# Performance work log

Measured on AMD Instinct MI355X. Metric: run time of the kernel, lower is better.

Reference implementation:

```python
import jax, jax.numpy as jnp
import numpy as np

N_NODES = 100000
N_EDGES = 1600000
IN_DIM = 128
HID = 64
NEG_SLOPE = 0.01  # F.leaky_relu default


def setup_inputs() -> dict:
    key = jax.random.key(0)
    ks = jax.random.split(key, 8)
    h = jax.random.normal(ks[0], (N_NODES, IN_DIM), dtype=jnp.float32)
    edge_index = jax.random.randint(ks[1], (2, N_EDGES), 0, N_NODES, dtype=jnp.int32)
    s1 = 1.0 / np.sqrt(IN_DIM)
    s2 = 1.0 / np.sqrt(HID)
    W1a = jax.random.normal(ks[2], (IN_DIM, HID), dtype=jnp.float32) * s1
    b1a = jnp.zeros((HID,), dtype=jnp.float32)
    W1b = jax.random.normal(ks[3], (HID, HID), dtype=jnp.float32) * s2
    b1b = jnp.zeros((HID,), dtype=jnp.float32)
    W2a = jax.random.normal(ks[4], (HID, HID), dtype=jnp.float32) * s2
    b2a = jnp.zeros((HID,), dtype=jnp.float32)
    W2b = jax.random.normal(ks[5], (HID, HID), dtype=jnp.float32) * s2
    b2b = jnp.zeros((HID,), dtype=jnp.float32)
    return dict(h=h, edge_index=edge_index, W1a=W1a, b1a=b1a, W1b=W1b, b1b=b1b,
                W2a=W2a, b2a=b2a, W2b=W2b, b2b=b2b)


def _gin_layer(h, src, dst, Wa, ba, Wb, bb):
    # sum aggregation over incoming edges: agg[v] = sum_{(u->v)} h[u]
    agg = jax.ops.segment_sum(h[src], dst, num_segments=N_NODES)
    z = h + agg  # (1 + eps) * h + agg, eps = 0 (learn_eps=False)
    z = jax.nn.relu(z @ Wa + ba) @ Wb + bb  # 2-layer MLP
    return jax.nn.leaky_relu(z, NEG_SLOPE)


def reference(h, edge_index, W1a, b1a, W1b, b1b, W2a, b2a, W2b, b2b):
    src, dst = edge_index[0], edge_index[1]
    h = _gin_layer(h, src, dst, W1a, b1a, W1b, b1b)
    h = _gin_layer(h, src, dst, W2a, b2a, W2b, b2b)
    return h
```

## Files before the change

### kernel.cpp

```cpp
#include <hip/hip_runtime.h>

#define IN_DIM 128
#define HID 64
#define NEG 0.01f
#define NBUCK 512
#define EPT 16

typedef unsigned int uint;
typedef unsigned short u16;
typedef __attribute__((ext_vector_type(8))) short s8v;
typedef __attribute__((ext_vector_type(4))) float f4v;

__device__ __forceinline__ float blo(uint u) { return __uint_as_float(u << 16); }
__device__ __forceinline__ float bhi(uint u) { return __uint_as_float(u & 0xffff0000u); }
__device__ __forceinline__ u16 bf16r(float x) {
    uint u = __float_as_uint(x);
    u = (u + 0x7fffu + ((u >> 16) & 1u)) >> 16;
    return (u16)u;
}
__device__ __forceinline__ uint bfpair(float a, float b) {
    uint ua = __float_as_uint(a), ub = __float_as_uint(b);
    ua = (ua + 0x7fffu + ((ua >> 16) & 1u)) >> 16;
    ub = (ub + 0x7fffu + ((ub >> 16) & 1u)) & 0xffff0000u;
    return ua | ub;
}
__device__ __forceinline__ s8v pack8(float4 x, float4 y) {
    uint4 qq = make_uint4(bfpair(x.x, x.y), bfpair(x.z, x.w),
                          bfpair(y.x, y.y), bfpair(y.z, y.w));
    return *reinterpret_cast<s8v*>(&qq);
}

__global__ __launch_bounds__(256) void prep_frags(const float* __restrict__ W1a,
                                                  const float* __restrict__ W1b,
                                                  const float* __restrict__ W2a,
                                                  const float* __restrict__ W2b,
                                                  u16* __restrict__ wf,
                                                  int* __restrict__ gcnt) {
    int t = threadIdx.x;
    for (int i = t; i < NBUCK; i += 256) gcnt[i] = 0;
    for (int task = t; task < 40 * 64; task += 256) {
        int f = task >> 6, l = task & 63;
        const float* W;
        int kt, nt;
        if (f < 16)      { W = W1a; kt = f & 3;        nt = f >> 2; }
        else if (f < 24) { W = W1b; kt = (f - 16) & 1; nt = (f - 16) >> 1; }
        else if (f < 32) { W = W2a; kt = (f - 24) & 1; nt = (f - 24) >> 1; }
        else             { W = W2b; kt = (f - 32) & 1; nt = (f - 32) >> 1; }
        int col = nt * 16 + (l & 15);
        int k0  = kt * 32 + (l >> 4) * 8;
        for (int j = 0; j < 8; ++j)
            wf[f * 512 + l * 8 + j] = bf16r(W[(k0 + j) * HID + col]);
    }
}

__global__ __launch_bounds__(256) void proj_hist(const float* __restrict__ h,
                                                 const u16* __restrict__ wf,
                                                 u16* __restrict__ pout, int M,
                                                 const int* __restrict__ dst,
                                                 int* __restrict__ gcnt,
                                                 int nE, int B, int histB) {
    if ((int)blockIdx.x < histB) {
        __shared__ int lc[NBUCK];
        for (int i = threadIdx.x; i < NBUCK; i += 256) lc[i] = 0;
        __syncthreads();
        int idx = blockIdx.x * 256 + threadIdx.x;
        int stride = histB * 256;
        for (int e = idx; e < nE; e += stride) atomicAdd(&lc[dst[e] >> 8], 1);
        __syncthreads();
        for (int i = threadIdx.x; i < B; i += 256) {
            int c = lc[i];
            if (c) atomicAdd(&gcnt[i], c);
        }
    } else {
        int wid = threadIdx.x >> 6, lane = threadIdx.x & 63;
        int lr = lane & 15, kg = lane >> 4;
        int node0 = ((int)blockIdx.x - histB) * 64 + wid * 16;
        s8v bfr[16];
#pragma unroll
        for (int f = 0; f < 16; ++f)
            bfr[f] = *reinterpret_cast<const s8v*>(wf + f * 512 + lane * 8);
        f4v zero = {0.f, 0.f, 0.f, 0.f};
        f4v acc[4] = {zero, zero, zero, zero};
        int nodeA = min(node0 + lr, M - 1);
        const float* hp = h + (size_t)nodeA * IN_DIM + kg * 8;
#pragma unroll
        for (int kt = 0; kt < 4; ++kt) {
            float4 x = *reinterpret_cast<const float4*>(hp + kt * 32);
            float4 y = *reinterpret_cast<const float4*>(hp + kt * 32 + 4);
            s8v afr = pack8(x, y);
#pragma unroll
            for (int nt = 0; nt < 4; ++nt)
                acc[nt] = __builtin_amdgcn_mfma_f32_16x16x32_bf16(afr, bfr[nt * 4 + kt], acc[nt], 0, 0, 0);
        }
#pragma unroll
        for (int jj = 0; jj < 4; ++jj) {
            int node = node0 + kg * 4 + jj;
            if (node < M) {
#pragma unroll
                for (int nt = 0; nt < 4; ++nt)
                    pout[(size_t)node * HID + nt * 16 + lr] = bf16r(acc[nt][jj]);
            }
        }
    }
}

__global__ __launch_bounds__(256) void coarse_scan(const int* __restrict__ gcnt,
                                                   int* __restrict__ bbase,
                                                   int* __restrict__ bcur) {
    __shared__ int sc[NBUCK];
    int t = threadIdx.x;
    sc[t] = gcnt[t];
    sc[t + 256] = gcnt[t + 256];
    __syncthreads();
    for (int off = 1; off < NBUCK; off <<= 1) {
        int x0 = sc[t], x1 = sc[t + 256];
        int y0 = (t >= off) ? sc[t - off] : 0;
        int y1 = (t + 256 >= off) ? sc[t + 256 - off] : 0;
        __syncthreads();
        sc[t] = x0 + y0;
        sc[t + 256] = x1 + y1;
        __syncthreads();
    }
    int e0 = (t == 0) ? 0 : sc[t - 1];
    int e1 = sc[t + 255];
    bbase[t] = e0;        bcur[t] = e0;
    bbase[t + 256] = e1;  bcur[t + 256] = e1;
}

__global__ __launch_bounds__(256) void partition(const int* __restrict__ src,
                                                 const int* __restrict__ dst,
                                                 int* __restrict__ bcur,
                                                 uint* __restrict__ ebuf,
                                                 int nE, int nRounds) {
    __shared__ int rcnt[NBUCK];
    __shared__ int chunk[NBUCK];
    int t = threadIdx.x;
    for (int r = blockIdx.x; r < nRounds; r += gridDim.x) {
        int base = r * (EPT * 256);
        for (int i = t; i < NBUCK; i += 256) rcnt[i] = 0;
        __syncthreads();
        uint pk[EPT];
        int rb[EPT];
#pragma unroll
        for (int j = 0; j < EPT; ++j) {
            int e = base + j * 256 + t;
            rb[j] = -1;
            if (e < nE) {
                int d = dst[e];
                int b = d >> 8;
                pk[j] = (uint)src[e] | ((uint)(d & 255) << 24);
                int rk = atomicAdd(&rcnt[b], 1);
                rb[j] = (rk << 9) | b;
            }
        }
        __syncthreads();
        for (int i = t; i < NBUCK; i += 256) {
            int c = rcnt[i];
            if (c) chunk[i] = atomicAdd(&bcur[i], c);
        }
        __syncthreads();
#pragma unroll
        for (int j = 0; j < EPT; ++j) {
            if (rb[j] >= 0) {
                int b = rb[j] & 511, rk = rb[j] >> 9;
                ebuf[chunk[b] + rk] = pk[j];
            }
        }
        __syncthreads();
    }
}

__global__ __launch_bounds__(256) void bucket_csr(const uint* __restrict__ ebuf,
                                                  const int* __restrict__ bbase,
                                                  const int* __restrict__ bcur,
                                                  int* __restrict__ rp,
                                                  int* __restrict__ ssrc,
                                                  int M, int nE) {
    __shared__ int cnt[256], sc[256], cur[256];
    int b = blockIdx.x, t = threadIdx.x;
    int ebeg = bbase[b], eend = bcur[b];
    cnt[t] = 0;
    __syncthreads();
    for (int e = ebeg + t; e < eend; e += 256) atomicAdd(&cnt[ebuf[e] >> 24], 1);
    __syncthreads();
    sc[t] = cnt[t];
    __syncthreads();
    for (int off = 1; off < 256; off <<= 1) {
        int x = sc[t];
        int y = (t >= off) ? sc[t - off] : 0;
        __syncthreads();
        sc[t] = x + y;
        __syncthreads();
    }
    int excl = (t == 0) ? 0 : sc[t - 1];
    int node = (b << 8) + t;
    if (node < M) rp[node] = ebeg + excl;
    if (b == 0 && t == 0) rp[M] = nE;
    cur[t] = excl;
    __syncthreads();
    for (int e = ebeg + t; e < eend; e += 256) {
        uint u = ebuf[e];
        int r = atomicAdd(&cur[u >> 24], 1);
        ssrc[ebeg + r] = (int)(u & 0x00ffffffu);
    }
}

__global__ __launch_bounds__(256, 8) void gather_z(const uint* __restrict__ pin,
                                                   const int* __restrict__ rp,
                                                   const int* __restrict__ ssrc,
                                                   const float* __restrict__ ba,
                                                   uint* __restrict__ zout, int M) {
    int lane = threadIdx.x & 63;
    int half = lane >> 5, col = lane & 31;
    int wave = (blockIdx.x * 256 + threadIdx.x) >> 6;
    int nW = gridDim.x * 4;
    for (int v = wave; v < M; v += nW) {
        int beg = rp[v], end = rp[v + 1];
        float f0 = 0.f, f1 = 0.f;
        for (int cb = beg; cb < end; cb += 64) {
            int n = min(64, end - cb);
            int eid = (lane < n) ? ssrc[cb + lane] : 0;
            int j = 0;
            for (; j + 16 <= n; j += 16) {
                int s0 = __shfl(eid, j + 0 + half);
                int s1 = __shfl(eid, j + 2 + half);
                int s2 = __shfl(eid, j + 4 + half);
                int s3 = __shfl(eid, j + 6 + half);
                int s4 = __shfl(eid, j + 8 + half);
                int s5 = __shfl(eid, j + 10 + half);
                int s6 = __shfl(eid, j + 12 + half);
                int s7 = __shfl(eid, j + 14 + half);
                uint u0 = pin[(size_t)s0 * 32 + col];
                uint u1 = pin[(size_t)s1 * 32 + col];
                uint u2 = pin[(size_t)s2 * 32 + col];
                uint u3 = pin[(size_t)s3 * 32 + col];
                uint u4 = pin[(size_t)s4 * 32 + col];
                uint u5 = pin[(size_t)s5 * 32 + col];
                uint u6 = pin[(size_t)s6 * 32 + col];
                uint u7 = pin[(size_t)s7 * 32 + col];
                f0 += (blo(u0) + blo(u1)) + (blo(u2) + blo(u3))
                    + (blo(u4) + blo(u5)) + (blo(u6) + blo(u7));
                f1 += (bhi(u0) + bhi(u1)) + (bhi(u2) + bhi(u3))
                    + (bhi(u4) + bhi(u5)) + (bhi(u6) + bhi(u7));
            }
            for (; j + 8 <= n; j += 8) {
                int s0 = __shfl(eid, j + 0 + half);
                int s1 = __shfl(eid, j + 2 + half);
                int s2 = __shfl(eid, j + 4 + half);
                int s3 = __shfl(eid, j + 6 + half);
                uint u0 = pin[(size_t)s0 * 32 + col];
                uint u1 = pin[(size_t)s1 * 32 + col];
                uint u2 = pin[(size_t)s2 * 32 + col];
                uint u3 = pin[(size_t)s3 * 32 + col];
                f0 += (blo(u0) + blo(u1)) + (blo(u2) + blo(u3));
                f1 += (bhi(u0) + bhi(u1)) + (bhi(u2) + bhi(u3));
            }
            for (; j < n; j += 2) {
                int idx = j + half;
                int s = __shfl(eid, idx);
                uint u = 0;
                if (idx < n) u = pin[(size_t)s * 32 + col];
                f0 += blo(u);
                f1 += bhi(u);
            }
        }
        f0 += __shfl_xor(f0, 32);
        f1 += __shfl_xor(f1, 32);
        uint us = pin[(size_t)v * 32 + col];
        f0 += blo(us);
        f1 += bhi(us);
        float2 vb = ((const float2*)ba)[col];
        f0 = fmaxf(f0 + vb.x, 0.f);
        f1 = fmaxf(f1 + vb.y, 0.f);
        if (lane < 32) zout[(size_t)v * 32 + col] = bfpair(f0, f1);
    }
}

template<bool HAS_NEXT>
__global__ __launch_bounds__(256) void mlp_mfma(const u16* __restrict__ zin,
                                                const u16* __restrict__ wfb,
                                                const float* __restrict__ bb,
                                                const u16* __restrict__ wfn,
                                                u16* __restrict__ pout,
                                                float* __restrict__ fout, int M) {
    int wid = threadIdx.x >> 6, lane = threadIdx.x & 63;
    int lr = lane & 15, kg = lane >> 4;
    int node0 = blockIdx.x * 64 + wid * 16;
    s8v bfr[8];
#pragma unroll
    for (int f = 0; f < 8; ++f)
        bfr[f] = *reinterpret_cast<const s8v*>(wfb + f * 512 + lane * 8);
    f4v zero = {0.f, 0.f, 0.f, 0.f};
    f4v acc[4] = {zero, zero, zero, zero};
    int nodeA = min(node0 + lr, M - 1);
    const u16* zp = zin + (size_t)nodeA * HID + kg * 8;
#pragma unroll
    for (int kt = 0; kt < 2; ++kt) {
        s8v afr = *reinterpret_cast<const s8v*>(zp + kt * 32);
#pragma unroll
        for (int nt = 0; nt < 4; ++nt)
            acc[nt] = __builtin_amdgcn_mfma_f32_16x16x32_bf16(afr, bfr[nt * 2 + kt], acc[nt], 0, 0, 0);
    }
    float h1[4][4];
#pragma unroll
    for (int nt = 0; nt < 4; ++nt) {
        float b = bb[nt * 16 + lr];
#pragma unroll
        for (int jj = 0; jj < 4; ++jj) {
            float v = acc[nt][jj] + b;
            h1[nt][jj] = (v > 0.f) ? v : v * NEG;
        }
    }
    if constexpr (!HAS_NEXT) {
#pragma unroll
        for (int jj = 0; jj < 4; ++jj) {
            int node = node0 + kg * 4 + jj;
            if (node < M) {
#pragma unroll
                for (int nt = 0; nt < 4; ++nt)
                    fout[(size_t)node * HID + nt * 16 + lr] = h1[nt][jj];
            }
        }
    } else {
        __shared__ float tls[4][16][68];
#pragma unroll
        for (int nt = 0; nt < 4; ++nt)
#pragma unroll
            for (int jj = 0; jj < 4; ++jj)
                tls[wid][kg * 4 + jj][nt * 16 + lr] = h1[nt][jj];
        s8v wfr[8];
#pragma unroll
        for (int f = 0; f < 8; ++f)
            wfr[f] = *reinterpret_cast<const s8v*>(wfn + f * 512 + lane * 8);
        f4v acc2[4] = {zero, zero, zero, zero};
#pragma unroll
        for (int kt = 0; kt < 2; ++kt) {
            float4 x = *reinterpret_cast<const float4*>(&tls[wid][lr][kt * 32 + kg * 8]);
            float4 y = *reinterpret_cast<const float4*>(&tls[wid][lr][kt * 32 + kg * 8 + 4]);
            s8v afr = pack8(x, y);
#pragma unroll
            for (int nt = 0; nt < 4; ++nt)
                acc2[nt] = __builtin_amdgcn_mfma_f32_16x16x32_bf16(afr, wfr[nt * 2 + kt], acc2[nt], 0, 0, 0);
        }
#pragma unroll
        for (int jj = 0; jj < 4; ++jj) {
            int node = node0 + kg * 4 + jj;
            if (node < M) {
#pragma unroll
                for (int nt = 0; nt < 4; ++nt)
                    pout[(size_t)node * HID + nt * 16 + lr] = bf16r(acc2[nt][jj]);
            }
        }
    }
}

extern "C" void kernel_launch(void* const* d_in, const int* in_sizes, int n_in,
                              void* d_out, int out_size, void* d_ws, size_t ws_size,
                              hipStream_t stream) {
    const float* h   = (const float*)d_in[0];
    const int*   ei  = (const int*)d_in[1];
    const float* W1a = (const float*)d_in[2];
    const float* b1a = (const float*)d_in[3];
    const float* W1b = (const float*)d_in[4];
    const float* b1b = (const float*)d_in[5];
    const float* W2a = (const float*)d_in[6];
    const float* b2a = (const float*)d_in[7];
    const float* W2b = (const float*)d_in[8];
    const float* b2b = (const float*)d_in[9];

    int M  = in_sizes[0] / IN_DIM;
    int nE = in_sizes[1] / 2;
    const int* src = ei;
    const int* dst = ei + nE;

    int B = (M + 255) >> 8;

    uint*  p1    = (uint*)d_ws;
    uint*  p2    = p1 + (size_t)M * 32;
    uint*  z     = p2 + (size_t)M * 32;
    int*   gcnt  = (int*)(z + (size_t)M * 32);
    int*   bbase = gcnt + NBUCK;
    int*   bcur  = bbase + NBUCK;
    int*   rp    = bcur + NBUCK;
    int*   ssrc  = rp + (M + 1);
    uint*  ebuf  = (uint*)(ssrc + nE);
    u16*   wf    = (u16*)(ebuf + nE);

    int gB = 2048;
    int mB = (M + 63) / 64;
    int histB = 160;
    int nRounds = (nE + EPT * 256 - 1) / (EPT * 256);

    prep_frags<<<1, 256, 0, stream>>>(W1a, W1b, W2a, W2b, wf, gcnt);

    proj_hist<<<histB + mB, 256, 0, stream>>>(h, wf, (u16*)p1, M, dst, gcnt, nE, B, histB);

    coarse_scan<<<1, 256, 0, stream>>>(gcnt, bbase, bcur);
    partition<<<nRounds, 256, 0, stream>>>(src, dst, bcur, ebuf, nE, nRounds);
    bucket_csr<<<B, 256, 0, stream>>>(ebuf, bbase, bcur, rp, ssrc, M, nE);

    gather_z<<<gB, 256, 0, stream>>>(p1, rp, ssrc, b1a, z, M);
    mlp_mfma<true><<<mB, 256, 0, stream>>>((const u16*)z, wf + 16 * 512, b1b, wf + 24 * 512,
                                           (u16*)p2, nullptr, M);
    gather_z<<<gB, 256, 0, stream>>>(p2, rp, ssrc, b2a, z, M);
    mlp_mfma<false><<<mB, 256, 0, stream>>>((const u16*)z, wf + 32 * 512, b2b, nullptr,
                                            nullptr, (float*)d_out, M);
}
```

Measured before the change: 163.6 us.

## Gather with 8 lanes per node using 16-byte loads instead of one wave per node

Restructures the CSR gather so each wave handles 8 nodes, with 8 lanes per node each loading a uint4 (8 bf16 features) per neighbor. Indices are read directly per lane instead of being staged and broadcast with shuffles. The grid grows to one thread per 8 features of every node rather than a grid-stride loop. This cuts shuffle overhead and per-wave serialization over low-degree nodes and issues wider loads, at the cost of divergence between nodes of different degree within a wave.

```diff
diff --git a/kernel.cpp b/kernel.cpp
--- a/kernel.cpp
+++ b/kernel.cpp
@@ -211,69 +211,56 @@
                                                    const float* __restrict__ ba,
                                                    uint* __restrict__ zout, int M) {
     int lane = threadIdx.x & 63;
-    int half = lane >> 5, col = lane & 31;
-    int wave = (blockIdx.x * 256 + threadIdx.x) >> 6;
-    int nW = gridDim.x * 4;
-    for (int v = wave; v < M; v += nW) {
-        int beg = rp[v], end = rp[v + 1];
-        float f0 = 0.f, f1 = 0.f;
-        for (int cb = beg; cb < end; cb += 64) {
-            int n = min(64, end - cb);
-            int eid = (lane < n) ? ssrc[cb + lane] : 0;
-            int j = 0;
-            for (; j + 16 <= n; j += 16) {
-                int s0 = __shfl(eid, j + 0 + half);
-                int s1 = __shfl(eid, j + 2 + half);
-                int s2 = __shfl(eid, j + 4 + half);
-                int s3 = __shfl(eid, j + 6 + half);
-                int s4 = __shfl(eid, j + 8 + half);
-                int s5 = __shfl(eid, j + 10 + half);
-                int s6 = __shfl(eid, j + 12 + half);
-                int s7 = __shfl(eid, j + 14 + half);
-                uint u0 = pin[(size_t)s0 * 32 + col];
-                uint u1 = pin[(size_t)s1 * 32 + col];
-                uint u2 = pin[(size_t)s2 * 32 + col];
-                uint u3 = pin[(size_t)s3 * 32 + col];
-                uint u4 = pin[(size_t)s4 * 32 + col];
-                uint u5 = pin[(size_t)s5 * 32 + col];
-                uint u6 = pin[(size_t)s6 * 32 + col];
-                uint u7 = pin[(size_t)s7 * 32 + col];
-                f0 += (blo(u0) + blo(u1)) + (blo(u2) + blo(u3))
-                    + (blo(u4) + blo(u5)) + (blo(u6) + blo(u7));
-                f1 += (bhi(u0) + bhi(u1)) + (bhi(u2) + bhi(u3))
-                    + (bhi(u4) + bhi(u5)) + (bhi(u6) + bhi(u7));
-            }
-            for (; j + 8 <= n; j += 8) {
-                int s0 = __shfl(eid, j + 0 + half);
-                int s1 = __shfl(eid, j + 2 + half);
-                int s2 = __shfl(eid, j + 4 + half);
-                int s3 = __shfl(eid, j + 6 + half);
-                uint u0 = pin[(size_t)s0 * 32 + col];
-                uint u1 = pin[(size_t)s1 * 32 + col];
-                uint u2 = pin[(size_t)s2 * 32 + col];
-                uint u3 = pin[(size_t)s3 * 32 + col];
-                f0 += (blo(u0) + blo(u1)) + (blo(u2) + blo(u3));
-                f1 += (bhi(u0) + bhi(u1)) + (bhi(u2) + bhi(u3));
-            }
-            for (; j < n; j += 2) {
-                int idx = j + half;
-                int s = __shfl(eid, idx);
-                uint u = 0;
-                if (idx < n) u = pin[(size_t)s * 32 + col];
-                f0 += blo(u);
-                f1 += bhi(u);
-            }
-        }
-        f0 += __shfl_xor(f0, 32);
-        f1 += __shfl_xor(f1, 32);
-        uint us = pin[(size_t)v * 32 + col];
-        f0 += blo(us);
-        f1 += bhi(us);
-        float2 vb = ((const float2*)ba)[col];
-        f0 = fmaxf(f0 + vb.x, 0.f);
-        f1 = fmaxf(f1 + vb.y, 0.f);
-        if (lane < 32) zout[(size_t)v * 32 + col] = bfpair(f0, f1);
-    }
+    int g = lane >> 3, q = lane & 7;
+    int w = (blockIdx.x * 256 + threadIdx.x) >> 6;
+    int v = w * 8 + g;
+    if (v >= M) return;
+    const uint4* pin4 = (const uint4*)pin;
+    int beg = rp[v], end = rp[v + 1];
+    uint4 u = pin4[(size_t)v * 8 + q];
+    float f0 = blo(u.x), f1 = bhi(u.x), f2 = blo(u.y), f3 = bhi(u.y);
+    float f4 = blo(u.z), f5 = bhi(u.z), f6 = blo(u.w), f7 = bhi(u.w);
+    int e = beg;
+    for (; e + 4 <= end; e += 4) {
+        int s0 = ssrc[e], s1 = ssrc[e + 1], s2 = ssrc[e + 2], s3 = ssrc[e + 3];
+        uint4 a = pin4[(size_t)s0 * 8 + q];
+        uint4 b = pin4[(size_t)s1 * 8 + q];
+        uint4 c = pin4[(size_t)s2 * 8 + q];
+        uint4 d = pin4[(size_t)s3 * 8 + q];
+        f0 += (blo(a.x) + blo(b.x)) + (blo(c.x) + blo(d.x));
+        f1 += (bhi(a.x) + bhi(b.x)) + (bhi(c.x) + bhi(d.x));
+        f2 += (blo(a.y) + blo(b.y)) + (blo(c.y) + blo(d.y));
+        f3 += (bhi(a.y) + bhi(b.y)) + (bhi(c.y) + bhi(d.y));
+        f4 += (blo(a.z) + blo(b.z)) + (blo(c.z) + blo(d.z));
+        f5 += (bhi(a.z) + bhi(b.z)) + (bhi(c.z) + bhi(d.z));
+        f6 += (blo(a.w) + blo(b.w)) + (blo(c.w) + blo(d.w));
+        f7 += (bhi(a.w) + bhi(b.w)) + (bhi(c.w) + bhi(d.w));
+    }
+    for (; e + 2 <= end; e += 2) {
+        int s0 = ssrc[e], s1 = ssrc[e + 1];
+        uint4 a = pin4[(size_t)s0 * 8 + q];
+        uint4 b = pin4[(size_t)s1 * 8 + q];
+        f0 += blo(a.x) + blo(b.x);  f1 += bhi(a.x) + bhi(b.x);
+        f2 += blo(a.y) + blo(b.y);  f3 += bhi(a.y) + bhi(b.y);
+        f4 += blo(a.z) + blo(b.z);  f5 += bhi(a.z) + bhi(b.z);
+        f6 += blo(a.w) + blo(b.w);  f7 += bhi(a.w) + bhi(b.w);
+    }
+    if (e < end) {
+        int s0 = ssrc[e];
+        uint4 a = pin4[(size_t)s0 * 8 + q];
+        f0 += blo(a.x);  f1 += bhi(a.x);
+        f2 += blo(a.y);  f3 += bhi(a.y);
+        f4 += blo(a.z);  f5 += bhi(a.z);
+        f6 += blo(a.w);  f7 += bhi(a.w);
+    }
+    const float4* ba4 = (const float4*)ba;
+    float4 b0 = ba4[q * 2], b1 = ba4[q * 2 + 1];
+    float r0 = fmaxf(f0 + b0.x, 0.f), r1 = fmaxf(f1 + b0.y, 0.f);
+    float r2 = fmaxf(f2 + b0.z, 0.f), r3 = fmaxf(f3 + b0.w, 0.f);
+    float r4 = fmaxf(f4 + b1.x, 0.f), r5 = fmaxf(f5 + b1.y, 0.f);
+    float r6 = fmaxf(f6 + b1.z, 0.f), r7 = fmaxf(f7 + b1.w, 0.f);
+    uint4 o = make_uint4(bfpair(r0, r1), bfpair(r2, r3), bfpair(r4, r5), bfpair(r6, r7));
+    ((uint4*)zout)[(size_t)v * 8 + q] = o;
 }
 
 template<bool HAS_NEXT>
@@ -386,8 +373,8 @@
     uint*  ebuf  = (uint*)(ssrc + nE);
     u16*   wf    = (u16*)(ebuf + nE);
 
-    int gB = 2048;
     int mB = (M + 63) / 64;
+    int gB = (M + 31) / 32;
     int histB = 160;
     int nRounds = (nE + EPT * 256 - 1) / (EPT * 256);
 
```

Measured after the change: 148.3 us. 1.1x faster.
